# Kernel tuning notes

Hardware: AMD Instinct MI355X
Metric: run time of the kernel (lower is better)

## Reference

```python
import jax, jax.numpy as jnp
import numpy as np

B, S, D, H = 8, 1500, 1024, 16
HD = D // H
DFF = 4 * D
EPS = 1e-5


def _xavier(key, shape):
    fan_in, fan_out = shape[1], shape[0]
    limit = float(np.sqrt(6.0 / (fan_in + fan_out)))
    return jax.random.uniform(key, shape, jnp.float32, -limit, limit)


def setup_inputs() -> dict:
    key = jax.random.key(0)
    ks = jax.random.split(key, 8)
    return {
        "hidden_states": jax.random.normal(ks[0], (B, S, D), jnp.float32),
        "Wq": _xavier(ks[1], (D, D)),
        "Wk": _xavier(ks[2], (D, D)),
        "Wv": _xavier(ks[3], (D, D)),
        "Wo": _xavier(ks[4], (D, D)),
        "W1": _xavier(ks[5], (DFF, D)),
        "b1": jnp.zeros((DFF,), jnp.float32),
        "W2": _xavier(ks[6], (D, DFF)),
        "b2": jnp.zeros((D,), jnp.float32),
        "ln1_g": jnp.ones((D,), jnp.float32),
        "ln1_b": jnp.zeros((D,), jnp.float32),
        "ln2_g": jnp.ones((D,), jnp.float32),
        "ln2_b": jnp.zeros((D,), jnp.float32),
    }


def _layernorm(x, g, b):
    mu = jnp.mean(x, axis=-1, keepdims=True)
    var = jnp.mean(jnp.square(x - mu), axis=-1, keepdims=True)
    return (x - mu) * jax.lax.rsqrt(var + EPS) * g + b


def reference(hidden_states, Wq, Wk, Wv, Wo, W1, b1, W2, b2, ln1_g, ln1_b, ln2_g, ln2_b):
    x = hidden_states
    residual = x
    h = _layernorm(x, ln1_g, ln1_b)
    # torch Linear: y = h @ W.T ; reshape to heads
    q = (h @ Wq.T).reshape(B, S, H, HD).transpose(0, 2, 1, 3) * (HD ** -0.5)
    k = (h @ Wk.T).reshape(B, S, H, HD).transpose(0, 2, 1, 3)
    v = (h @ Wv.T).reshape(B, S, H, HD).transpose(0, 2, 1, 3)
    scores = jnp.einsum('bhqd,bhkd->bhqk', q, k)
    attn = jax.nn.softmax(scores.astype(jnp.float32), axis=-1).astype(h.dtype)
    ctx = jnp.einsum('bhqk,bhkd->bhqd', attn, v)
    ctx = ctx.transpose(0, 2, 1, 3).reshape(B, S, D)
    x = residual + ctx @ Wo.T
    residual = x
    h = _layernorm(x, ln2_g, ln2_b)
    ffn = jax.nn.gelu(h @ W1.T + b1, approximate=False) @ W2.T + b2
    return residual + ffn
```

## Files before the change

kernel.cpp:

```cpp
#include <hip/hip_runtime.h>
#include <hip/hip_bf16.h>
#include <cstdint>
#include <cstddef>

#define B_    8
#define S_    1500
#define D_    1024
#define H_    16
#define HD_   64
#define DFF_  4096
#define M_    12000
#define VTS_  1536

typedef __bf16 bf16;
typedef __attribute__((ext_vector_type(8))) __bf16 bf16x8;
typedef __attribute__((ext_vector_type(4))) float f32x4;

#define MFMA16(a, b, c) __builtin_amdgcn_mfma_f32_16x16x32_bf16((a), (b), (c), 0, 0, 0)

static __device__ __forceinline__ void gload16(const void* g, void* l) {
  __builtin_amdgcn_global_load_lds(
      (const __attribute__((address_space(1))) void*)(uintptr_t)g,
      (__attribute__((address_space(3))) void*)(uintptr_t)l, 16, 0, 0);
}

static __device__ __forceinline__ unsigned short f2bu(float v) {
  bf16 h = (bf16)v;
  union { bf16 h; unsigned short u; } c;
  c.h = h;
  return c.u;
}

static constexpr size_t HSZ      = (size_t)M_ * D_ * 2;
static constexpr size_t H_OFF    = 0;
static constexpr size_t WQ_OFF   = H_OFF + HSZ;
static constexpr size_t WK_OFF   = WQ_OFF + (size_t)D_ * D_ * 2;
static constexpr size_t WV_OFF   = WK_OFF + (size_t)D_ * D_ * 2;
static constexpr size_t WO_OFF   = WV_OFF + (size_t)D_ * D_ * 2;
static constexpr size_t Q_OFF    = WO_OFF + (size_t)D_ * D_ * 2;
static constexpr size_t K_OFF    = Q_OFF + HSZ;
static constexpr size_t VT_OFF   = K_OFF + HSZ;
static constexpr size_t W1_OFF   = VT_OFF + (size_t)128 * 64 * VTS_ * 2;
static constexpr size_t W2_OFF   = W1_OFF + (size_t)DFF_ * D_ * 2;
static constexpr size_t WS_BASE  = W2_OFF + (size_t)DFF_ * D_ * 2;
static constexpr size_t H2B_OFF  = WS_BASE;
static constexpr size_t NEED_BIG = WS_BASE + HSZ;
static constexpr size_t H2F_OFF  = VT_OFF;
static constexpr size_t ACT_OFF  = 0;

__launch_bounds__(256)
__global__ void cvt_bf16(const float* __restrict__ src, bf16* __restrict__ dst, int n) {
  int i = (blockIdx.x * 256 + threadIdx.x) * 4;
  if (i < n) {
    float4 f = *(const float4*)(src + i);
    dst[i + 0] = (bf16)f.x;
    dst[i + 1] = (bf16)f.y;
    dst[i + 2] = (bf16)f.z;
    dst[i + 3] = (bf16)f.w;
  }
}

__launch_bounds__(256)
__global__ void ln_fused(const float* __restrict__ x, const float* __restrict__ g,
                         const float* __restrict__ bb, bf16* __restrict__ out) {
  const int row = blockIdx.x;
  const int t = threadIdx.x;
  const float4 xv = *(const float4*)(x + (size_t)row * D_ + t * 4);
  float s  = xv.x + xv.y + xv.z + xv.w;
  float s2 = xv.x * xv.x + xv.y * xv.y + xv.z * xv.z + xv.w * xv.w;
#pragma unroll
  for (int m = 32; m >= 1; m >>= 1) {
    s  += __shfl_xor(s, m);
    s2 += __shfl_xor(s2, m);
  }
  __shared__ float red[8];
  const int w = t >> 6;
  if ((t & 63) == 0) { red[w] = s; red[4 + w] = s2; }
  __syncthreads();
  s  = red[0] + red[1] + red[2] + red[3];
  s2 = red[4] + red[5] + red[6] + red[7];
  const float mu  = s * (1.0f / D_);
  const float var = s2 * (1.0f / D_) - mu * mu;
  const float rs  = rsqrtf(var + 1e-5f);
  const float4 gv = *(const float4*)(g + t * 4);
  const float4 bv = *(const float4*)(bb + t * 4);
  bf16* o = out + (size_t)row * D_ + t * 4;
  o[0] = (bf16)((xv.x - mu) * rs * gv.x + bv.x);
  o[1] = (bf16)((xv.y - mu) * rs * gv.y + bv.y);
  o[2] = (bf16)((xv.z - mu) * rs * gv.z + bv.z);
  o[3] = (bf16)((xv.w - mu) * rs * gv.w + bv.w);
}

template <int EPI>
__launch_bounds__(1024, 4)
__global__ void gemm256(const bf16* __restrict__ A, const bf16* __restrict__ Bw,
                        int M, int N, int K,
                        bf16* __restrict__ outB, float* outF,
                        const float* __restrict__ bias, const float* resid,
                        bf16* __restrict__ outQ, bf16* __restrict__ outK2,
                        bf16* __restrict__ outV) {
  __shared__ bf16 a_lds[2][256 * 64];
  __shared__ bf16 b_lds[2][256 * 64];

  const int t = threadIdx.x;
  const int lane = t & 63, wid = t >> 6;
  const int wm = wid >> 2, wn = wid & 3;
  const int l15 = lane & 15, hi = lane >> 4;
  const int l7 = l15 & 7;
  const int mrow0 = blockIdx.x * 256;
  const int ncol0 = blockIdx.y * 256;

  const int rl = t >> 3;
  const int sc8 = ((t & 7) ^ (rl & 7)) << 3;
  unsigned offA[2], offB[2];
#pragma unroll
  for (int j = 0; j < 2; ++j) {
    int gr = mrow0 + j * 128 + rl; gr = gr < M ? gr : M - 1;
    offA[j] = (unsigned)gr * (unsigned)K + (unsigned)sc8;
    offB[j] = (unsigned)(ncol0 + j * 128 + rl) * (unsigned)K + (unsigned)sc8;
  }

  f32x4 acc[4][4] = {};

  const int NT = K >> 6;

  {
    char* ad = (char*)&a_lds[0][0];
    char* bd = (char*)&b_lds[0][0];
    gload16(A + offA[0], ad + t * 16);
    gload16(A + offA[1], ad + 16384 + t * 16);
    gload16(Bw + offB[0], bd + t * 16);
    gload16(Bw + offB[1], bd + 16384 + t * 16);
  }
  __syncthreads();

  int buf = 0;
  for (int tt = 0; tt < NT; ++tt) {
    if (tt + 1 < NT) {
      const unsigned k1 = (unsigned)(tt + 1) << 6;
      char* ad = (char*)&a_lds[buf ^ 1][0];
      char* bd = (char*)&b_lds[buf ^ 1][0];
      gload16(A + offA[0] + k1, ad + t * 16);
      gload16(A + offA[1] + k1, ad + 16384 + t * 16);
      gload16(Bw + offB[0] + k1, bd + t * 16);
      gload16(Bw + offB[1] + k1, bd + 16384 + t * 16);
    }

    const bf16* al = &a_lds[buf][0];
    const bf16* bl = &b_lds[buf][0];
#pragma unroll
    for (int kk = 0; kk < 2; ++kk) {
      bf16x8 af_[4], bf_[4];
      const int cc = ((kk * 4 + hi) ^ l7) << 3;
#pragma unroll
      for (int m = 0; m < 4; ++m)
        af_[m] = *(const bf16x8*)&al[(wm * 64 + m * 16 + l15) * 64 + cc];
#pragma unroll
      for (int n = 0; n < 4; ++n)
        bf_[n] = *(const bf16x8*)&bl[(wn * 64 + n * 16 + l15) * 64 + cc];
      __builtin_amdgcn_s_setprio(1);
#pragma unroll
      for (int m = 0; m < 4; ++m)
#pragma unroll
        for (int n = 0; n < 4; ++n)
          acc[m][n] = MFMA16(af_[m], bf_[n], acc[m][n]);
      __builtin_amdgcn_s_setprio(0);
    }

    __syncthreads();
    buf ^= 1;
  }

  const int r0 = hi * 4;

  if constexpr (EPI == 5) {
    const int mm = blockIdx.y >> 2;
    const int nloc0 = (blockIdx.y & 3) * 256;
    if (mm == 2) {
#pragma unroll
      for (int m = 0; m < 4; ++m) {
        int row0 = mrow0 + wm * 64 + m * 16 + r0;
        if (row0 < M) {
          int bb2 = row0 / 1500;
          int s = row0 - bb2 * 1500;
#pragma unroll
          for (int n = 0; n < 4; ++n) {
            int f = nloc0 + wn * 64 + n * 16 + l15;
            size_t a = ((size_t)(bb2 * 16 + (f >> 6)) * 64 + (f & 63)) * VTS_ + s;
            ushort4 pk;
            pk.x = f2bu(acc[m][n][0]);
            pk.y = f2bu(acc[m][n][1]);
            pk.z = f2bu(acc[m][n][2]);
            pk.w = f2bu(acc[m][n][3]);
            *reinterpret_cast<ushort4*>((unsigned short*)outV + a) = pk;
          }
        }
      }
    } else {
      bf16* dst = (mm == 0) ? outQ : outK2;
      const float sc = (mm == 0) ? 0.18033688011112042f : 1.0f;
#pragma unroll
      for (int m = 0; m < 4; ++m) {
#pragma unroll
        for (int n = 0; n < 4; ++n) {
          int col = nloc0 + wn * 64 + n * 16 + l15;
#pragma unroll
          for (int r = 0; r < 4; ++r) {
            int row = mrow0 + wm * 64 + m * 16 + r0 + r;
            if (row < M) dst[(size_t)row * D_ + col] = (bf16)(acc[m][n][r] * sc);
          }
        }
      }
    }
    return;
  }

#pragma unroll
  for (int m = 0; m < 4; ++m) {
#pragma unroll
    for (int n = 0; n < 4; ++n) {
      int col = ncol0 + wn * 64 + n * 16 + l15;
#pragma unroll
      for (int r = 0; r < 4; ++r) {
        int row = mrow0 + wm * 64 + m * 16 + r0 + r;
        if (row < M) {
          float v = acc[m][n][r];
          if constexpr (EPI == 2) {
            float xg = v + bias[col];
            v = 0.5f * xg * (1.0f + erff(xg * 0.70710678118654752f));
            outB[(size_t)row * N + col] = (bf16)v;
          }
          if constexpr (EPI == 3) {
            v += resid[(size_t)row * N + col];
            if (bias) v += bias[col];
            outF[(size_t)row * N + col] = v;
          }
        }
      }
    }
  }
}

template <int EPI>
__launch_bounds__(256)
__global__ void gemm_bt(const bf16* __restrict__ A, const bf16* __restrict__ Bw,
                        int M, int N, int K,
                        bf16* __restrict__ outB, float* outF,
                        const float* __restrict__ bias, const float* resid,
                        float scale) {
  __shared__ bf16 a_lds[128 * 64];
  __shared__ bf16 b_lds[128 * 64];
  const int t = threadIdx.x;
  const int lane = t & 63, wid = t >> 6;
  const int wr = wid >> 1, wc = wid & 1;
  const int mrow0 = blockIdx.x * 128;
  const int ncol0 = blockIdx.y * 128;
  const int l15 = lane & 15;
  const int khi = (lane >> 4) << 3;

  f32x4 acc[4][4] = {};

  for (int k0 = 0; k0 < K; k0 += 64) {
#pragma unroll
    for (int i = 0; i < 4; ++i) {
      int idx = i * 2048 + t * 8;
      int row = idx >> 6, col = idx & 63;
      int gr = mrow0 + row;
      gr = gr < M ? gr : M - 1;
      gload16(A + (size_t)gr * K + (k0 + col), (char*)a_lds + idx * 2);
    }
#pragma unroll
    for (int i = 0; i < 4; ++i) {
      int idx = i * 2048 + t * 8;
      int row = idx >> 6, col = idx & 63;
      gload16(Bw + (size_t)(ncol0 + row) * K + (k0 + col), (char*)b_lds + idx * 2);
    }
    __syncthreads();
#pragma unroll
    for (int kk = 0; kk < 2; ++kk) {
      bf16x8 af[4], bfv[4];
#pragma unroll
      for (int m = 0; m < 4; ++m)
        af[m] = *(const bf16x8*)&a_lds[(wr * 64 + m * 16 + l15) * 64 + kk * 32 + khi];
#pragma unroll
      for (int n = 0; n < 4; ++n)
        bfv[n] = *(const bf16x8*)&b_lds[(wc * 64 + n * 16 + l15) * 64 + kk * 32 + khi];
#pragma unroll
      for (int m = 0; m < 4; ++m)
#pragma unroll
        for (int n = 0; n < 4; ++n)
          acc[m][n] = MFMA16(af[m], bfv[n], acc[m][n]);
    }
    __syncthreads();
  }

  const int r0 = (lane >> 4) << 2;
#pragma unroll
  for (int m = 0; m < 4; ++m) {
#pragma unroll
    for (int n = 0; n < 4; ++n) {
      int col = ncol0 + wc * 64 + n * 16 + l15;
#pragma unroll
      for (int r = 0; r < 4; ++r) {
        int row = mrow0 + wr * 64 + m * 16 + r0 + r;
        if (row < M) {
          float v = acc[m][n][r];
          if constexpr (EPI == 2) {
            float xg = v + bias[col];
            v = 0.5f * xg * (1.0f + erff(xg * 0.70710678118654752f));
          }
          if constexpr (EPI == 3) {
            v += resid[(size_t)row * N + col];
            if (bias) v += bias[col];
            outF[(size_t)row * N + col] = v;
          } else {
            outB[(size_t)row * N + col] = (bf16)v;
          }
        }
      }
    }
  }
}

__launch_bounds__(256, 4)
__global__ void attn_fwd6(const bf16* __restrict__ q, const bf16* __restrict__ kg,
                          const bf16* __restrict__ vt, bf16* __restrict__ cx) {
  __shared__ bf16 k_lds[2][64 * 64];
  __shared__ bf16 v_lds[2][64 * 64];
  __shared__ bf16 p_lds[4][16 * 64];

  const int t = threadIdx.x;
  const int lane = t & 63, w = t >> 6;
  const int L = blockIdx.x;
  const int wu = (L & 7) * 384 + (L >> 3);
  const int bh = wu / 24;
  const int qt = wu - bh * 24;
  const int l15 = lane & 15;
  const int hi = lane >> 4;
  const int khi = hi << 3;

  const size_t hoff = ((size_t)(bh >> 4) * S_) * D_ + (size_t)(bh & 15) * HD_;
  const bf16* qh = q + hoff;
  const bf16* kh = kg + hoff;
  const bf16* vh = vt + (size_t)bh * (64 * VTS_);

  const int st_r0 = t >> 3;
  const int st_c  = t & 7;

  int qr = qt * 64 + w * 16 + l15;
  int qrc = qr < S_ ? qr : S_ - 1;
  const bf16x8 qf0 = *(const bf16x8*)(qh + (size_t)qrc * D_ + khi);
  const bf16x8 qf1 = *(const bf16x8*)(qh + (size_t)qrc * D_ + 32 + khi);

  f32x4 oacc[4] = {};
  float mrun[4], lrun[4];
#pragma unroll
  for (int r = 0; r < 4; ++r) { mrun[r] = -1e30f; lrun[r] = 0.f; }

  bf16* pw = &p_lds[w][0];
  const int NT = (S_ + 63) / 64;
  const float THR = 11.5415605f;

#pragma unroll
  for (int i = 0; i < 2; ++i) {
    int row = i * 32 + st_r0;
    int sc = st_c ^ (row & 7);
    int key = row < S_ ? row : S_ - 1;
    gload16(kh + (size_t)key * D_ + sc * 8, (char*)&k_lds[0][0] + (i * 2048 + t * 8) * 2);
    gload16(vh + (size_t)row * VTS_ + sc * 8, (char*)&v_lds[0][0] + (i * 2048 + t * 8) * 2);
  }
  __syncthreads();

  int buf = 0;
  for (int kt = 0; kt < NT; ++kt) {
    if (kt + 1 < NT) {
      int kb = (kt + 1) * 64;
#pragma unroll
      for (int i = 0; i < 2; ++i) {
        int row = i * 32 + st_r0;
        int sc = st_c ^ (row & 7);
        int key = kb + row;
        key = key < S_ ? key : S_ - 1;
        gload16(kh + (size_t)key * D_ + sc * 8,
                (char*)&k_lds[buf ^ 1][0] + (i * 2048 + t * 8) * 2);
        gload16(vh + (size_t)row * VTS_ + kb + sc * 8,
                (char*)&v_lds[buf ^ 1][0] + (i * 2048 + t * 8) * 2);
      }
    }

    float pv[4][4];
    __builtin_amdgcn_s_setprio(1);
#pragma unroll
    for (int nb = 0; nb < 4; ++nb) {
      int krow = nb * 16 + l15;
      f32x4 z = {};
      z = MFMA16(qf0, *(const bf16x8*)&k_lds[buf][krow * 64 + ((hi ^ (l15 & 7)) << 3)], z);
      z = MFMA16(qf1, *(const bf16x8*)&k_lds[buf][krow * 64 + (((4 + hi) ^ (l15 & 7)) << 3)], z);
#pragma unroll
      for (int r = 0; r < 4; ++r) pv[nb][r] = z[r];
    }
    __builtin_amdgcn_s_setprio(0);

    if (kt == NT - 1) {
#pragma unroll
      for (int nb = 0; nb < 4; ++nb) {
        bool cvld = (kt * 64 + nb * 16 + l15) < S_;
#pragma unroll
        for (int r = 0; r < 4; ++r) pv[nb][r] = cvld ? pv[nb][r] : -1e30f;
      }
    }

    float lmax[4];
    bool ok = true;
#pragma unroll
    for (int r = 0; r < 4; ++r) {
      lmax[r] = fmaxf(fmaxf(pv[0][r], pv[1][r]), fmaxf(pv[2][r], pv[3][r]));
      ok = ok && (lmax[r] <= mrun[r] + THR);
    }
    if (!__all(ok)) {
#pragma unroll
      for (int r = 0; r < 4; ++r) {
        float mx = lmax[r];
        mx = fmaxf(mx, __shfl_xor(mx, 1));
        mx = fmaxf(mx, __shfl_xor(mx, 2));
        mx = fmaxf(mx, __shfl_xor(mx, 4));
        mx = fmaxf(mx, __shfl_xor(mx, 8));
        float mnew = fmaxf(mrun[r], mx);
        float corr = exp2f(mrun[r] - mnew);
        lrun[r] *= corr;
        mrun[r] = mnew;
#pragma unroll
        for (int db = 0; db < 4; ++db) oacc[db][r] *= corr;
      }
    }

#pragma unroll
    for (int r = 0; r < 4; ++r) {
      float p0 = exp2f(pv[0][r] - mrun[r]);
      float p1 = exp2f(pv[1][r] - mrun[r]);
      float p2 = exp2f(pv[2][r] - mrun[r]);
      float p3 = exp2f(pv[3][r] - mrun[r]);
      pv[0][r] = p0; pv[1][r] = p1; pv[2][r] = p2; pv[3][r] = p3;
      lrun[r] += (p0 + p1) + (p2 + p3);
    }

#pragma unroll
    for (int nb = 0; nb < 4; ++nb) {
#pragma unroll
      for (int r = 0; r < 4; ++r) {
        int prow = hi * 4 + r;
        int pcol = (nb * 16 + l15) ^ ((prow & 7) << 3);
        pw[prow * 64 + pcol] = (bf16)pv[nb][r];
      }
    }

    __builtin_amdgcn_s_setprio(1);
#pragma unroll
    for (int kk = 0; kk < 2; ++kk) {
      bf16x8 pf = *(const bf16x8*)&pw[l15 * 64 + (((kk * 4 + hi) ^ (l15 & 7)) << 3)];
#pragma unroll
      for (int db = 0; db < 4; ++db) {
        int vrow = db * 16 + l15;
        bf16x8 vf = *(const bf16x8*)&v_lds[buf][vrow * 64 + (((kk * 4 + hi) ^ (l15 & 7)) << 3)];
        oacc[db] = MFMA16(pf, vf, oacc[db]);
      }
    }
    __builtin_amdgcn_s_setprio(0);

    __syncthreads();
    buf ^= 1;
  }

#pragma unroll
  for (int r = 0; r < 4; ++r) {
    float ps = lrun[r];
    ps += __shfl_xor(ps, 1);
    ps += __shfl_xor(ps, 2);
    ps += __shfl_xor(ps, 4);
    ps += __shfl_xor(ps, 8);
    int qrow = qt * 64 + w * 16 + hi * 4 + r;
    if (qrow < S_) {
      float inv = 1.0f / ps;
#pragma unroll
      for (int db = 0; db < 4; ++db)
        cx[hoff + (size_t)qrow * D_ + db * 16 + l15] = (bf16)(oacc[db][r] * inv);
    }
  }
}

extern "C" void kernel_launch(void* const* d_in, const int* in_sizes, int n_in,
                              void* d_out, int out_size, void* d_ws, size_t ws_size,
                              hipStream_t stream) {
  const float* x   = (const float*)d_in[0];
  const float* Wq  = (const float*)d_in[1];
  const float* Wk  = (const float*)d_in[2];
  const float* Wv  = (const float*)d_in[3];
  const float* Wo  = (const float*)d_in[4];
  const float* W1  = (const float*)d_in[5];
  const float* b1  = (const float*)d_in[6];
  const float* W2  = (const float*)d_in[7];
  const float* b2  = (const float*)d_in[8];
  const float* g1  = (const float*)d_in[9];
  const float* be1 = (const float*)d_in[10];
  const float* g2  = (const float*)d_in[11];
  const float* be2 = (const float*)d_in[12];
  float* out = (float*)d_out;

  char* ws = (char*)d_ws;
  bf16* h_b   = (bf16*)(ws + H_OFF);
  bf16* wq_b  = (bf16*)(ws + WQ_OFF);
  bf16* wk_b  = (bf16*)(ws + WK_OFF);
  bf16* wv_b  = (bf16*)(ws + WV_OFF);
  bf16* wo_b  = (bf16*)(ws + WO_OFF);
  bf16* w1_b  = (bf16*)(ws + W1_OFF);
  bf16* w2_b  = (bf16*)(ws + W2_OFF);
  bf16* q_b   = (bf16*)(ws + Q_OFF);
  bf16* k_b   = (bf16*)(ws + K_OFF);
  bf16* vt_b  = (bf16*)(ws + VT_OFF);
  bf16* act_b = (bf16*)(ws + ACT_OFF);
  bf16* ctx_b = h_b;

  const bool big = ws_size >= NEED_BIG;
  bf16* h2_b = (bf16*)(ws + (big ? H2B_OFF : H2F_OFF));

  cvt_bf16<<<(D_ * D_) / 1024, 256, 0, stream>>>(Wq, wq_b, D_ * D_);
  cvt_bf16<<<(D_ * D_) / 1024, 256, 0, stream>>>(Wk, wk_b, D_ * D_);
  cvt_bf16<<<(D_ * D_) / 1024, 256, 0, stream>>>(Wv, wv_b, D_ * D_);
  cvt_bf16<<<(D_ * D_) / 1024, 256, 0, stream>>>(Wo, wo_b, D_ * D_);
  cvt_bf16<<<(DFF_ * D_) / 1024, 256, 0, stream>>>(W1, w1_b, DFF_ * D_);
  cvt_bf16<<<(DFF_ * D_) / 1024, 256, 0, stream>>>(W2, w2_b, DFF_ * D_);

  ln_fused<<<M_, 256, 0, stream>>>(x, g1, be1, h_b);

  gemm256<5><<<dim3((M_ + 255) / 256, 12), 1024, 0, stream>>>(
      h_b, wq_b, M_, 3072, D_, nullptr, nullptr, nullptr, nullptr, q_b, k_b, vt_b);

  attn_fwd6<<<3072, 256, 0, stream>>>(q_b, k_b, vt_b, ctx_b);

  gemm256<3><<<dim3((M_ + 255) / 256, 4), 1024, 0, stream>>>(
      ctx_b, wo_b, M_, D_, D_, nullptr, out, nullptr, x, nullptr, nullptr, nullptr);

  ln_fused<<<M_, 256, 0, stream>>>(out, g2, be2, h2_b);

  if (big) {
    gemm256<2><<<dim3((M_ + 255) / 256, DFF_ / 256), 1024, 0, stream>>>(
        h2_b, w1_b, M_, DFF_, D_, act_b, nullptr, b1, nullptr,
        nullptr, nullptr, nullptr);
    gemm256<3><<<dim3((M_ + 255) / 256, D_ / 256), 1024, 0, stream>>>(
        act_b, w2_b, M_, D_, DFF_, nullptr, out, b2, out,
        nullptr, nullptr, nullptr);
  } else {
    for (int c = 0; c < 3; ++c) {
      int r0c = c * 4000;
      int nr = 4000;
      gemm256<2><<<dim3((nr + 255) / 256, DFF_ / 256), 1024, 0, stream>>>(
          h2_b + (size_t)r0c * D_, w1_b, nr, DFF_, D_, act_b, nullptr, b1, nullptr,
          nullptr, nullptr, nullptr);
      gemm_bt<3><<<dim3((nr + 127) / 128, D_ / 128), 256, 0, stream>>>(
          act_b, w2_b, nr, D_, DFF_, nullptr, out + (size_t)r0c * D_, b2,
          out + (size_t)r0c * D_, 0.f);
    }
  }
}
```

Before: 643.3 us.

## Widen attention blocks to 128 query rows with 8 waves sharing K/V tiles

The attention kernel now uses 512-thread blocks with 8 waves, each covering 16 query rows, so one block handles 128 queries per head instead of 64. Each K/V tile staged in LDS is reused by twice as many waves, and every thread issues a single async load per tile, which halves K/V global traffic and staging work per query. The cost is fewer blocks (1536), a larger per-block LDS footprint, and higher occupancy demands from launch bounds of 6, which may pressure registers. The last query tile also wastes more padded rows.

Result: slower. 669.8 us (+4.1%).

```diff
diff --git a/kernel.cpp b/kernel.cpp
--- a/kernel.cpp
+++ b/kernel.cpp
@@ -322,19 +322,19 @@
   }
 }
 
-__launch_bounds__(256, 4)
-__global__ void attn_fwd6(const bf16* __restrict__ q, const bf16* __restrict__ kg,
+__launch_bounds__(512, 6)
+__global__ void attn_fwd7(const bf16* __restrict__ q, const bf16* __restrict__ kg,
                           const bf16* __restrict__ vt, bf16* __restrict__ cx) {
   __shared__ bf16 k_lds[2][64 * 64];
   __shared__ bf16 v_lds[2][64 * 64];
-  __shared__ bf16 p_lds[4][16 * 64];
+  __shared__ bf16 p_lds[8][16 * 64];
 
   const int t = threadIdx.x;
   const int lane = t & 63, w = t >> 6;
   const int L = blockIdx.x;
-  const int wu = (L & 7) * 384 + (L >> 3);
-  const int bh = wu / 24;
-  const int qt = wu - bh * 24;
+  const int wu = (L & 7) * 192 + (L >> 3);
+  const int bh = wu / 12;
+  const int qt = wu - bh * 12;
   const int l15 = lane & 15;
   const int hi = lane >> 4;
   const int khi = hi << 3;
@@ -344,10 +344,11 @@
   const bf16* kh = kg + hoff;
   const bf16* vh = vt + (size_t)bh * (64 * VTS_);
 
-  const int st_r0 = t >> 3;
-  const int st_c  = t & 7;
-
-  int qr = qt * 64 + w * 16 + l15;
+  const int st_r = t >> 3;
+  const int st_c = t & 7;
+  const int st_sc = (st_c ^ (st_r & 7)) * 8;
+
+  int qr = qt * 128 + w * 16 + l15;
   int qrc = qr < S_ ? qr : S_ - 1;
   const bf16x8 qf0 = *(const bf16x8*)(qh + (size_t)qrc * D_ + khi);
   const bf16x8 qf1 = *(const bf16x8*)(qh + (size_t)qrc * D_ + 32 + khi);
@@ -361,13 +362,10 @@
   const int NT = (S_ + 63) / 64;
   const float THR = 11.5415605f;
 
-#pragma unroll
-  for (int i = 0; i < 2; ++i) {
-    int row = i * 32 + st_r0;
-    int sc = st_c ^ (row & 7);
-    int key = row < S_ ? row : S_ - 1;
-    gload16(kh + (size_t)key * D_ + sc * 8, (char*)&k_lds[0][0] + (i * 2048 + t * 8) * 2);
-    gload16(vh + (size_t)row * VTS_ + sc * 8, (char*)&v_lds[0][0] + (i * 2048 + t * 8) * 2);
+  {
+    int key = st_r < S_ ? st_r : S_ - 1;
+    gload16(kh + (size_t)key * D_ + st_sc, (char*)&k_lds[0][0] + t * 16);
+    gload16(vh + (size_t)st_r * VTS_ + st_sc, (char*)&v_lds[0][0] + t * 16);
   }
   __syncthreads();
 
@@ -375,17 +373,12 @@
   for (int kt = 0; kt < NT; ++kt) {
     if (kt + 1 < NT) {
       int kb = (kt + 1) * 64;
-#pragma unroll
-      for (int i = 0; i < 2; ++i) {
-        int row = i * 32 + st_r0;
-        int sc = st_c ^ (row & 7);
-        int key = kb + row;
-        key = key < S_ ? key : S_ - 1;
-        gload16(kh + (size_t)key * D_ + sc * 8,
-                (char*)&k_lds[buf ^ 1][0] + (i * 2048 + t * 8) * 2);
-        gload16(vh + (size_t)row * VTS_ + kb + sc * 8,
-                (char*)&v_lds[buf ^ 1][0] + (i * 2048 + t * 8) * 2);
-      }
+      int key = kb + st_r;
+      key = key < S_ ? key : S_ - 1;
+      gload16(kh + (size_t)key * D_ + st_sc,
+              (char*)&k_lds[buf ^ 1][0] + t * 16);
+      gload16(vh + (size_t)st_r * VTS_ + kb + st_sc,
+              (char*)&v_lds[buf ^ 1][0] + t * 16);
     }
 
     float pv[4][4];
@@ -478,7 +471,7 @@
     ps += __shfl_xor(ps, 2);
     ps += __shfl_xor(ps, 4);
     ps += __shfl_xor(ps, 8);
-    int qrow = qt * 64 + w * 16 + hi * 4 + r;
+    int qrow = qt * 128 + w * 16 + hi * 4 + r;
     if (qrow < S_) {
       float inv = 1.0f / ps;
 #pragma unroll
@@ -535,7 +528,7 @@
   gemm256<5><<<dim3((M_ + 255) / 256, 12), 1024, 0, stream>>>(
       h_b, wq_b, M_, 3072, D_, nullptr, nullptr, nullptr, nullptr, q_b, k_b, vt_b);
 
-  attn_fwd6<<<3072, 256, 0, stream>>>(q_b, k_b, vt_b, ctx_b);
+  attn_fwd7<<<1536, 512, 0, stream>>>(q_b, k_b, vt_b, ctx_b);
 
   gemm256<3><<<dim3((M_ + 255) / 256, 4), 1024, 0, stream>>>(
       ctx_b, wo_b, M_, D_, D_, nullptr, out, nullptr, x, nullptr, nullptr, nullptr);
```
